# Performance work log

Measured on AMD Instinct MI355X. Metric: run time of the kernel, lower is better.

The kernel has to match this reference:

```python
import jax, jax.numpy as jnp
import numpy as np
import math

Q, D, M_KEYS, U, DELTA = 32, 64, 4096, 64, 16
B = 1024
GAMMA_ALPHA = 0.1
EPS = 1e-12


def _l2norm(v, axis):
    n = jnp.sqrt(jnp.sum(v * v, axis=axis, keepdims=True))
    return v / jnp.maximum(n, EPS)


def setup_inputs() -> dict:
    key = jax.random.key(0)
    kx, kk, km = jax.random.split(key, 3)
    x = jax.random.normal(kx, (B, D), dtype=jnp.float32)
    K = jax.random.normal(kk, (Q, M_KEYS, D), dtype=jnp.float32)
    M = jax.random.normal(km, (Q, M_KEYS, U), dtype=jnp.float32)
    return {"x": x, "K": K, "M": M}


def reference(x, K, M):
    b = x.shape[0]
    # psi: identity projection onto key space + L2 normalization
    x_bd = _l2norm(x, axis=1)                      # [b, d]
    # keys are L2-normalized along the key dimension (F.normalize, dim=2)
    Kn = _l2norm(K, axis=2)                        # [q, m, d]
    # per-neuron key matching: [b, q, m]
    responses_bqm = jnp.einsum("bd,qmd->bqm", x_bd, Kn)
    # top-delta attention responses (sorted, largest)
    top_resp_bqk, top_idx_bqk = jax.lax.top_k(responses_bqm, DELTA)
    # temperature-scaled softmax over the top-delta responses
    top_alpha_bqk = jax.nn.softmax(
        (GAMMA_ALPHA / math.sqrt(D)) * top_resp_bqk, axis=2
    )
    # gather the top-delta memory units per (batch, neuron): [b, q, k, u]
    q_idx = jnp.arange(Q)[None, :, None]           # [1, q, 1]
    top_M_bqku = M[q_idx, top_idx_bqk]             # advanced indexing gather
    # softmax-weighted combine: [b, q, u]
    W_bqu = jnp.einsum("bqk,bqku->bqu", top_alpha_bqk, top_M_bqku)
    return W_bqu
```

## Files before the change

### kernel.cpp

```cpp
#include <hip/hip_runtime.h>
#include <math.h>

#define QN 32
#define DN 64
#define MN 4096
#define UN 64
#define BN 1024
#define NDELTA 16
#define SEGS 2
#define SEGK (MN / SEGS)
#define SURV_CAP 64
#define THETA 0.27f
#define BAND  8e-3f

typedef short v8s __attribute__((ext_vector_type(8)));
typedef float v4f __attribute__((ext_vector_type(4)));

static __device__ __forceinline__ unsigned short f2bf(float f) {
    unsigned int u = __float_as_uint(f);
    unsigned int r = (u + 0x7FFF + ((u >> 16) & 1)) >> 16;
    return (unsigned short)r;
}

#define NKBLK ((QN * MN) / 16)
__global__ __launch_bounds__(256) void k_prep(const float* __restrict__ K,
                                              const float* __restrict__ x,
                                              float* __restrict__ rinvK,
                                              float* __restrict__ rinvx,
                                              unsigned short* __restrict__ Khat,
                                              unsigned short* __restrict__ xhat) {
    const int tid = threadIdx.x;
    const bool isK = blockIdx.x < NKBLK;
    const int rb   = isK ? blockIdx.x : (blockIdx.x - NKBLK);
    const int row  = rb * 16 + (tid >> 4);
    const int sub  = tid & 15;
    const float* src = isK ? K : x;
    float* rdst      = isK ? rinvK : rinvx;
    unsigned short* hdst = isK ? Khat : xhat;

    const float4* r4 = (const float4*)(src + (size_t)row * DN);
    float4 v = r4[sub];
    float ss = v.x * v.x + v.y * v.y + v.z * v.z + v.w * v.w;
    ss += __shfl_xor(ss, 1, 16);
    ss += __shfl_xor(ss, 2, 16);
    ss += __shfl_xor(ss, 4, 16);
    ss += __shfl_xor(ss, 8, 16);
    const float rinv = 1.0f / fmaxf(sqrtf(ss), 1e-12f);
    if (sub == 0) rdst[row] = rinv;
    ushort4 o;
    o.x = f2bf(v.x * rinv); o.y = f2bf(v.y * rinv);
    o.z = f2bf(v.z * rinv); o.w = f2bf(v.w * rinv);
    *(ushort4*)(hdst + (size_t)row * DN + sub * 4) = o;
}

__global__ __launch_bounds__(256, 4) void k_prefsel(
        const unsigned short* __restrict__ Khat,
        const unsigned short* __restrict__ xhat,
        unsigned int* __restrict__ cand2,
        int* __restrict__ cnt2) {
    __shared__ unsigned short sK[2][64][72];

    const int tid  = threadIdx.x;
    const int w    = tid >> 6;
    const int lane = tid & 63;

    const int d    = blockIdx.x;
    const int xcd  = d & 7;
    const int j    = d >> 3;
    const int g    = xcd + ((j >> 4) << 3);
    const int i    = j & 15;
    const int q    = g >> 1;
    const int seg  = g & 1;
    const int b0   = i * 64 + w * 16;

    const int col  = lane & 15;
    const int gg   = lane >> 4;

    const v8s* xp = (const v8s*)(xhat + (size_t)(b0 + col) * DN + gg * 8);
    const v8s xb0 = xp[0];
    const v8s xb1 = xp[4];

    const unsigned short* Kq16 = Khat + ((size_t)q * MN + seg * SEGK) * DN;
    const unsigned long long colmask = 0x0001000100010001ull << col;
    const size_t rowoff = (((size_t)(b0 + col) * QN + q) * SEGS + seg) * SURV_CAP;
    int cnt = 0;

    const int r0i = tid >> 3;
    const int oi  = (tid & 7) * 8;
    uint4 p0 = *(const uint4*)(Kq16 + (size_t)r0i * DN + oi);
    uint4 p1 = *(const uint4*)(Kq16 + (size_t)(32 + r0i) * DN + oi);
    int cur = 0;

    const int NST = SEGK / 64;
    for (int st = 0; st < NST; ++st) {
        *(uint4*)(&sK[cur][r0i][oi]) = p0;
        *(uint4*)(&sK[cur][32 + r0i][oi]) = p1;
        __syncthreads();
        if (st < NST - 1) {
            p0 = *(const uint4*)(Kq16 + (size_t)((st + 1) * 64 + r0i) * DN + oi);
            p1 = *(const uint4*)(Kq16 + (size_t)((st + 1) * 64 + 32 + r0i) * DN + oi);
        }

#pragma unroll
        for (int t2 = 0; t2 < 4; ++t2) {
            const unsigned short* arow = &sK[cur][t2 * 16 + col][0];
            const v8s a0 = *(const v8s*)(arow + gg * 8);
            const v8s a1 = *(const v8s*)(arow + gg * 8 + 32);
            v4f acc = {0.f, 0.f, 0.f, 0.f};
            acc = __builtin_amdgcn_mfma_f32_16x16x32_bf16(a0, xb0, acc, 0, 0, 0);
            acc = __builtin_amdgcn_mfma_f32_16x16x32_bf16(a1, xb1, acc, 0, 0, 0);
            const int keybase = seg * SEGK + st * 64 + t2 * 16 + gg * 4;
#pragma unroll
            for (int r = 0; r < 4; ++r) {
                const bool qual = acc[r] > THETA;
                const unsigned long long mm = __ballot(qual);
                if (mm) {
                    const unsigned long long mc = mm & colmask;
                    const int rank = __builtin_amdgcn_mbcnt_hi(
                        (unsigned int)(mc >> 32),
                        __builtin_amdgcn_mbcnt_lo((unsigned int)mc, 0));
                    const int inc = __popcll(mc);
                    if (qual) {
                        const int pos = cnt + rank;
                        if (pos < SURV_CAP)
                            cand2[rowoff + pos] =
                                (unsigned int)(keybase + r) |
                                ((unsigned int)f2bf(acc[r]) << 16);
                    }
                    cnt += inc;
                }
            }
        }
        cur ^= 1;
    }

    if (gg == 0)
        cnt2[((b0 + col) * QN + q) * SEGS + seg] = cnt < SURV_CAP ? cnt : SURV_CAP;
}

__global__ __launch_bounds__(256) void k_rescore7(
        const float* __restrict__ x,
        const float* __restrict__ K,
        const float* __restrict__ rinvx,
        const float* __restrict__ rinvK,
        const unsigned int* __restrict__ cand2,
        const int* __restrict__ cnt2,
        const float* __restrict__ Mm,
        float* __restrict__ out) {
    __shared__ float2 slist[4][NDELTA];

    const int tid  = threadIdx.x;
    const int lane = tid & 63;
    const int w    = tid >> 6;
    const unsigned long long below = (1ull << lane) - 1ull;

    const int d    = blockIdx.x;
    const int xcd  = d & 7;
    const int j    = d >> 3;
    const int q    = xcd + ((j >> 8) << 3);
    const int b    = (j & 255) * 4 + w;
    const int p    = b * QN + q;

    const int n0 = cnt2[p * SEGS + 0];
    const int n1 = cnt2[p * SEGS + 1];
    const unsigned int* cp = cand2 + (size_t)p * SEGS * SURV_CAP;
    const unsigned int eraw  = cp[lane];
    const unsigned int eraw2 = cp[SURV_CAP + lane];
    const float rx = rinvx[b];

    if (lane < NDELTA) slist[w][lane] = make_float2(0.f, 0.f);

    const bool va = lane < n0;
    const bool vb = lane < n1;
    const int key  = (int)(eraw  & 0xFFFFu);
    const int key2 = (int)(eraw2 & 0xFFFFu);
    const float m  = va ? __uint_as_float(eraw  & 0xFFFF0000u) : -INFINITY;
    const float m2 = vb ? __uint_as_float(eraw2 & 0xFFFF0000u) : -INFINITY;

    float lo = 0.25f, bh = 0.60f;
#pragma unroll
    for (int it = 0; it < 7; ++it) {
        const float tm = 0.5f * (lo + bh);
        const int c = __popcll(__ballot(m > tm)) + __popcll(__ballot(m2 > tm));
        if (c >= NDELTA) lo = tm; else bh = tm;
    }

    const bool hi  = m  > lo + BAND;
    const bool hi2 = m2 > lo + BAND;
    const bool bd  = va && !hi  && (m  >= lo - BAND);
    const bool bd2 = vb && !hi2 && (m2 >= lo - BAND);
    const unsigned long long bhi  = __ballot(hi);
    const unsigned long long bhi2 = __ballot(hi2);
    const int n_hi0 = __popcll(bhi);
    const int n_hi  = n_hi0 + __popcll(bhi2);
    const int need  = NDELTA - n_hi;

    const float4* xrow = (const float4*)(x + (size_t)b * DN);
    const float* Kq  = K + (size_t)q * MN * DN;
    const float* rKq = rinvK + (size_t)q * MN;

    float f = -INFINITY, g2 = -INFINITY;
    if (bd) {
        const float4* kr = (const float4*)(Kq + (size_t)key * DN);
        float a0 = 0.f, a1 = 0.f, a2 = 0.f, a3 = 0.f;
#pragma unroll
        for (int i = 0; i < 16; ++i) {
            const float4 xv = xrow[i];
            const float4 kv = kr[i];
            a0 = fmaf(kv.x, xv.x, a0);
            a1 = fmaf(kv.y, xv.y, a1);
            a2 = fmaf(kv.z, xv.z, a2);
            a3 = fmaf(kv.w, xv.w, a3);
        }
        f = ((a0 + a1) + (a2 + a3)) * (rx * rKq[key]);
    }
    const unsigned long long bbd2 = __ballot(bd2);
    if (bbd2) {
        if (bd2) {
            const float4* kr = (const float4*)(Kq + (size_t)key2 * DN);
            float a0 = 0.f, a1 = 0.f, a2 = 0.f, a3 = 0.f;
#pragma unroll
            for (int i = 0; i < 16; ++i) {
                const float4 xv = xrow[i];
                const float4 kv = kr[i];
                a0 = fmaf(kv.x, xv.x, a0);
                a1 = fmaf(kv.y, xv.y, a1);
                a2 = fmaf(kv.z, xv.z, a2);
                a3 = fmaf(kv.w, xv.w, a3);
            }
            g2 = ((a0 + a1) + (a2 + a3)) * (rx * rKq[key2]);
        }
    }

    int rkf = 0, rkf2 = 0;
    unsigned long long t1m = __ballot(bd);
    while (t1m) {
        const int t = __ffsll(t1m) - 1; t1m &= t1m - 1;
        const float ft = __shfl(f, t);
        const int   kt = __shfl(key, t);
        rkf  += (ft > f  || (ft == f  && kt < key )) ? 1 : 0;
        rkf2 += (ft > g2 || (ft == g2 && kt < key2)) ? 1 : 0;
    }
    unsigned long long t2m = bbd2;
    while (t2m) {
        const int t = __ffsll(t2m) - 1; t2m &= t2m - 1;
        const float ft = __shfl(g2, t);
        const int   kt = __shfl(key2, t);
        rkf  += (ft > f  || (ft == f  && kt < key )) ? 1 : 0;
        rkf2 += (ft > g2 || (ft == g2 && kt < key2)) ? 1 : 0;
    }

    const float SM_SCALE = (float)(0.1 / 8.0);
    if (hi)
        slist[w][__popcll(bhi & below)] =
            make_float2(__expf(m * SM_SCALE) , __int_as_float(key));
    if (hi2)
        slist[w][n_hi0 + __popcll(bhi2 & below)] =
            make_float2(__expf(m2 * SM_SCALE), __int_as_float(key2));
    if (bd && rkf < need)
        slist[w][n_hi + rkf] =
            make_float2(__expf(f * SM_SCALE) , __int_as_float(key));
    if (bd2 && rkf2 < need)
        slist[w][n_hi + rkf2] =
            make_float2(__expf(g2 * SM_SCALE), __int_as_float(key2));

    const float2 mine = slist[w][lane & 15];
    const float* Mq = Mm + (size_t)q * MN * UN;
    float ssum = 0.f;
    float acc = 0.f;
#pragma unroll
    for (int t = 0; t < NDELTA; ++t) {
        const float e  = __shfl(mine.x, t);
        const int   id = __float_as_int(__shfl(mine.y, t));
        ssum += e;
        acc = fmaf(e, Mq[(size_t)id * UN + lane], acc);
    }
    const float rs = ssum > 0.f ? 1.0f / ssum : 0.f;
    out[(size_t)p * UN + lane] = acc * rs;
}

extern "C" void kernel_launch(void* const* d_in, const int* in_sizes, int n_in,
                              void* d_out, int out_size, void* d_ws, size_t ws_size,
                              hipStream_t stream) {
    const float* x  = (const float*)d_in[0];
    const float* K  = (const float*)d_in[1];
    const float* Mm = (const float*)d_in[2];
    float* out = (float*)d_out;

    char* wsb = (char*)d_ws;
    float* rinvK = (float*)wsb;                   wsb += (size_t)QN * MN * 4;
    float* rinvx = (float*)wsb;                   wsb += (size_t)BN * 4;
    int*   cnt2  = (int*)wsb;                     wsb += (size_t)BN * QN * SEGS * 4;
    unsigned short* Khat = (unsigned short*)wsb;  wsb += (size_t)QN * MN * DN * 2;
    unsigned short* xhat = (unsigned short*)wsb;  wsb += (size_t)BN * DN * 2;
    unsigned int* cand2 = (unsigned int*)wsb;

    k_prep    <<<dim3(NKBLK + BN / 16), 256, 0, stream>>>(K, x, rinvK, rinvx,
                                                          Khat, xhat);
    k_prefsel <<<dim3(1024), 256, 0, stream>>>(Khat, xhat, cand2, cnt2);
    k_rescore7<<<dim3((BN * QN) / 4), 256, 0, stream>>>(x, K, rinvx, rinvK,
                                                        cand2, cnt2, Mm, out);
}
```

Baseline: 230.5 us.

## Fuse prefilter and rescore kernels, keeping candidate lists in shared memory

Merges the bf16 MFMA prefilter and the exact rescore/gather kernels into one kernel. Each block now scans all 4096 keys of a neuron for 64 batch rows and keeps up to 128 candidates per row in LDS, so the global candidate and count buffers and one launch go away. The cost is half as many blocks (512) and a large LDS footprint (about 32KB for candidates), which lowers occupancy. The rescore work is also serialized, with each wave looping over 16 rows, so parallelism and latency hiding may drop.

```diff
diff --git a/kernel.cpp b/kernel.cpp
--- a/kernel.cpp
+++ b/kernel.cpp
@@ -7,9 +7,7 @@
 #define UN 64
 #define BN 1024
 #define NDELTA 16
-#define SEGS 2
-#define SEGK (MN / SEGS)
-#define SURV_CAP 64
+#define CAP 128
 #define THETA 0.27f
 #define BAND  8e-3f
 
@@ -53,36 +51,40 @@
     *(ushort4*)(hdst + (size_t)row * DN + sub * 4) = o;
 }
 
-__global__ __launch_bounds__(256, 4) void k_prefsel(
+__global__ __launch_bounds__(256) void k_fused(
         const unsigned short* __restrict__ Khat,
         const unsigned short* __restrict__ xhat,
-        unsigned int* __restrict__ cand2,
-        int* __restrict__ cnt2) {
+        const float* __restrict__ x,
+        const float* __restrict__ K,
+        const float* __restrict__ rinvx,
+        const float* __restrict__ rinvK,
+        const float* __restrict__ Mm,
+        float* __restrict__ out) {
     __shared__ unsigned short sK[2][64][72];
+    __shared__ unsigned int clist[64][CAP];
+    __shared__ float2 slist[4][NDELTA];
 
     const int tid  = threadIdx.x;
     const int w    = tid >> 6;
     const int lane = tid & 63;
 
-    const int d    = blockIdx.x;
-    const int xcd  = d & 7;
-    const int j    = d >> 3;
-    const int g    = xcd + ((j >> 4) << 3);
-    const int i    = j & 15;
-    const int q    = g >> 1;
-    const int seg  = g & 1;
-    const int b0   = i * 64 + w * 16;
-
-    const int col  = lane & 15;
-    const int gg   = lane >> 4;
+    const int d   = blockIdx.x;
+    const int xcd = d & 7;
+    const int j   = d >> 3;
+    const int q   = xcd + ((j >> 4) << 3);
+    const int i   = j & 15;
+    const int b0  = i * 64 + w * 16;
+
+    const int col = lane & 15;
+    const int gg  = lane >> 4;
 
     const v8s* xp = (const v8s*)(xhat + (size_t)(b0 + col) * DN + gg * 8);
     const v8s xb0 = xp[0];
     const v8s xb1 = xp[4];
 
-    const unsigned short* Kq16 = Khat + ((size_t)q * MN + seg * SEGK) * DN;
+    const unsigned short* Kq16 = Khat + (size_t)q * MN * DN;
     const unsigned long long colmask = 0x0001000100010001ull << col;
-    const size_t rowoff = (((size_t)(b0 + col) * QN + q) * SEGS + seg) * SURV_CAP;
+    const int lb0 = w * 16 + col;
     int cnt = 0;
 
     const int r0i = tid >> 3;
@@ -91,7 +93,7 @@
     uint4 p1 = *(const uint4*)(Kq16 + (size_t)(32 + r0i) * DN + oi);
     int cur = 0;
 
-    const int NST = SEGK / 64;
+    const int NST = MN / 64;
     for (int st = 0; st < NST; ++st) {
         *(uint4*)(&sK[cur][r0i][oi]) = p0;
         *(uint4*)(&sK[cur][32 + r0i][oi]) = p1;
@@ -109,7 +111,7 @@
             v4f acc = {0.f, 0.f, 0.f, 0.f};
             acc = __builtin_amdgcn_mfma_f32_16x16x32_bf16(a0, xb0, acc, 0, 0, 0);
             acc = __builtin_amdgcn_mfma_f32_16x16x32_bf16(a1, xb1, acc, 0, 0, 0);
-            const int keybase = seg * SEGK + st * 64 + t2 * 16 + gg * 4;
+            const int keybase = st * 64 + t2 * 16 + gg * 4;
 #pragma unroll
             for (int r = 0; r < 4; ++r) {
                 const bool qual = acc[r] > THETA;
@@ -122,8 +124,8 @@
                     const int inc = __popcll(mc);
                     if (qual) {
                         const int pos = cnt + rank;
-                        if (pos < SURV_CAP)
-                            cand2[rowoff + pos] =
+                        if (pos < CAP)
+                            clist[lb0][pos] =
                                 (unsigned int)(keybase + r) |
                                 ((unsigned int)f2bf(acc[r]) << 16);
                     }
@@ -134,149 +136,133 @@
         cur ^= 1;
     }
 
-    if (gg == 0)
-        cnt2[((b0 + col) * QN + q) * SEGS + seg] = cnt < SURV_CAP ? cnt : SURV_CAP;
-}
-
-__global__ __launch_bounds__(256) void k_rescore7(
-        const float* __restrict__ x,
-        const float* __restrict__ K,
-        const float* __restrict__ rinvx,
-        const float* __restrict__ rinvK,
-        const unsigned int* __restrict__ cand2,
-        const int* __restrict__ cnt2,
-        const float* __restrict__ Mm,
-        float* __restrict__ out) {
-    __shared__ float2 slist[4][NDELTA];
-
-    const int tid  = threadIdx.x;
-    const int lane = tid & 63;
-    const int w    = tid >> 6;
-    const unsigned long long below = (1ull << lane) - 1ull;
-
-    const int d    = blockIdx.x;
-    const int xcd  = d & 7;
-    const int j    = d >> 3;
-    const int q    = xcd + ((j >> 8) << 3);
-    const int b    = (j & 255) * 4 + w;
-    const int p    = b * QN + q;
-
-    const int n0 = cnt2[p * SEGS + 0];
-    const int n1 = cnt2[p * SEGS + 1];
-    const unsigned int* cp = cand2 + (size_t)p * SEGS * SURV_CAP;
-    const unsigned int eraw  = cp[lane];
-    const unsigned int eraw2 = cp[SURV_CAP + lane];
-    const float rx = rinvx[b];
-
-    if (lane < NDELTA) slist[w][lane] = make_float2(0.f, 0.f);
-
-    const bool va = lane < n0;
-    const bool vb = lane < n1;
-    const int key  = (int)(eraw  & 0xFFFFu);
-    const int key2 = (int)(eraw2 & 0xFFFFu);
-    const float m  = va ? __uint_as_float(eraw  & 0xFFFF0000u) : -INFINITY;
-    const float m2 = vb ? __uint_as_float(eraw2 & 0xFFFF0000u) : -INFINITY;
-
-    float lo = 0.25f, bh = 0.60f;
-#pragma unroll
-    for (int it = 0; it < 7; ++it) {
-        const float tm = 0.5f * (lo + bh);
-        const int c = __popcll(__ballot(m > tm)) + __popcll(__ballot(m2 > tm));
-        if (c >= NDELTA) lo = tm; else bh = tm;
-    }
-
-    const bool hi  = m  > lo + BAND;
-    const bool hi2 = m2 > lo + BAND;
-    const bool bd  = va && !hi  && (m  >= lo - BAND);
-    const bool bd2 = vb && !hi2 && (m2 >= lo - BAND);
-    const unsigned long long bhi  = __ballot(hi);
-    const unsigned long long bhi2 = __ballot(hi2);
-    const int n_hi0 = __popcll(bhi);
-    const int n_hi  = n_hi0 + __popcll(bhi2);
-    const int need  = NDELTA - n_hi;
-
-    const float4* xrow = (const float4*)(x + (size_t)b * DN);
     const float* Kq  = K + (size_t)q * MN * DN;
     const float* rKq = rinvK + (size_t)q * MN;
-
-    float f = -INFINITY, g2 = -INFINITY;
-    if (bd) {
-        const float4* kr = (const float4*)(Kq + (size_t)key * DN);
-        float a0 = 0.f, a1 = 0.f, a2 = 0.f, a3 = 0.f;
-#pragma unroll
-        for (int i = 0; i < 16; ++i) {
-            const float4 xv = xrow[i];
-            const float4 kv = kr[i];
-            a0 = fmaf(kv.x, xv.x, a0);
-            a1 = fmaf(kv.y, xv.y, a1);
-            a2 = fmaf(kv.z, xv.z, a2);
-            a3 = fmaf(kv.w, xv.w, a3);
-        }
-        f = ((a0 + a1) + (a2 + a3)) * (rx * rKq[key]);
-    }
-    const unsigned long long bbd2 = __ballot(bd2);
-    if (bbd2) {
-        if (bd2) {
-            const float4* kr = (const float4*)(Kq + (size_t)key2 * DN);
+    const float* Mq  = Mm + (size_t)q * MN * UN;
+    const unsigned long long below = (1ull << lane) - 1ull;
+    const float SM_SCALE = (float)(0.1 / 8.0);
+
+#pragma unroll 1
+    for (int it = 0; it < 16; ++it) {
+        const int bb = b0 + it;
+        const int lb = w * 16 + it;
+        const int p  = bb * QN + q;
+
+        int n = __shfl(cnt, it);
+        n = n < CAP ? n : CAP;
+        const int n0 = n < 64 ? n : 64;
+        const int n1 = n - n0;
+
+        const unsigned int eraw  = clist[lb][lane];
+        const unsigned int eraw2 = clist[lb][64 + lane];
+        const float rx = rinvx[bb];
+
+        if (lane < NDELTA) slist[w][lane] = make_float2(0.f, 0.f);
+
+        const bool va = lane < n0;
+        const bool vb = lane < n1;
+        const int key  = (int)(eraw  & 0xFFFFu);
+        const int key2 = (int)(eraw2 & 0xFFFFu);
+        const float m  = va ? __uint_as_float(eraw  & 0xFFFF0000u) : -INFINITY;
+        const float m2 = vb ? __uint_as_float(eraw2 & 0xFFFF0000u) : -INFINITY;
+
+        float lo = 0.25f, bh = 0.60f;
+#pragma unroll
+        for (int s = 0; s < 7; ++s) {
+            const float tm = 0.5f * (lo + bh);
+            const int c = __popcll(__ballot(m > tm)) + __popcll(__ballot(m2 > tm));
+            if (c >= NDELTA) lo = tm; else bh = tm;
+        }
+
+        const bool hi  = m  > lo + BAND;
+        const bool hi2 = m2 > lo + BAND;
+        const bool bd  = va && !hi  && (m  >= lo - BAND);
+        const bool bd2 = vb && !hi2 && (m2 >= lo - BAND);
+        const unsigned long long bhi  = __ballot(hi);
+        const unsigned long long bhi2 = __ballot(hi2);
+        const int n_hi0 = __popcll(bhi);
+        const int n_hi  = n_hi0 + __popcll(bhi2);
+        const int need  = NDELTA - n_hi;
+
+        const float4* xrow = (const float4*)(x + (size_t)bb * DN);
+
+        float f = -INFINITY, g2 = -INFINITY;
+        if (bd) {
+            const float4* kr = (const float4*)(Kq + (size_t)key * DN);
             float a0 = 0.f, a1 = 0.f, a2 = 0.f, a3 = 0.f;
 #pragma unroll
-            for (int i = 0; i < 16; ++i) {
-                const float4 xv = xrow[i];
-                const float4 kv = kr[i];
+            for (int k4 = 0; k4 < 16; ++k4) {
+                const float4 xv = xrow[k4];
+                const float4 kv = kr[k4];
                 a0 = fmaf(kv.x, xv.x, a0);
                 a1 = fmaf(kv.y, xv.y, a1);
                 a2 = fmaf(kv.z, xv.z, a2);
                 a3 = fmaf(kv.w, xv.w, a3);
             }
-            g2 = ((a0 + a1) + (a2 + a3)) * (rx * rKq[key2]);
-        }
+            f = ((a0 + a1) + (a2 + a3)) * (rx * rKq[key]);
+        }
+        const unsigned long long bbd2 = __ballot(bd2);
+        if (bbd2) {
+            if (bd2) {
+                const float4* kr = (const float4*)(Kq + (size_t)key2 * DN);
+                float a0 = 0.f, a1 = 0.f, a2 = 0.f, a3 = 0.f;
+#pragma unroll
+                for (int k4 = 0; k4 < 16; ++k4) {
+                    const float4 xv = xrow[k4];
+                    const float4 kv = kr[k4];
+                    a0 = fmaf(kv.x, xv.x, a0);
+                    a1 = fmaf(kv.y, xv.y, a1);
+                    a2 = fmaf(kv.z, xv.z, a2);
+                    a3 = fmaf(kv.w, xv.w, a3);
+                }
+                g2 = ((a0 + a1) + (a2 + a3)) * (rx * rKq[key2]);
+            }
+        }
+
+        int rkf = 0, rkf2 = 0;
+        unsigned long long t1m = __ballot(bd);
+        while (t1m) {
+            const int t = __ffsll(t1m) - 1; t1m &= t1m - 1;
+            const float ft = __shfl(f, t);
+            const int   kt = __shfl(key, t);
+            rkf  += (ft > f  || (ft == f  && kt < key )) ? 1 : 0;
+            rkf2 += (ft > g2 || (ft == g2 && kt < key2)) ? 1 : 0;
+        }
+        unsigned long long t2m = bbd2;
+        while (t2m) {
+            const int t = __ffsll(t2m) - 1; t2m &= t2m - 1;
+            const float ft = __shfl(g2, t);
+            const int   kt = __shfl(key2, t);
+            rkf  += (ft > f  || (ft == f  && kt < key )) ? 1 : 0;
+            rkf2 += (ft > g2 || (ft == g2 && kt < key2)) ? 1 : 0;
+        }
+
+        if (hi)
+            slist[w][__popcll(bhi & below)] =
+                make_float2(__expf(m * SM_SCALE) , __int_as_float(key));
+        if (hi2)
+            slist[w][n_hi0 + __popcll(bhi2 & below)] =
+                make_float2(__expf(m2 * SM_SCALE), __int_as_float(key2));
+        if (bd && rkf < need)
+            slist[w][n_hi + rkf] =
+                make_float2(__expf(f * SM_SCALE) , __int_as_float(key));
+        if (bd2 && rkf2 < need)
+            slist[w][n_hi + rkf2] =
+                make_float2(__expf(g2 * SM_SCALE), __int_as_float(key2));
+
+        const float2 mine = slist[w][lane & 15];
+        float ssum = 0.f;
+        float acc = 0.f;
+#pragma unroll
+        for (int t = 0; t < NDELTA; ++t) {
+            const float e  = __shfl(mine.x, t);
+            const int   id = __float_as_int(__shfl(mine.y, t));
+            ssum += e;
+            acc = fmaf(e, Mq[(size_t)id * UN + lane], acc);
+        }
+        const float rs = ssum > 0.f ? 1.0f / ssum : 0.f;
+        out[(size_t)p * UN + lane] = acc * rs;
     }
-
-    int rkf = 0, rkf2 = 0;
-    unsigned long long t1m = __ballot(bd);
-    while (t1m) {
-        const int t = __ffsll(t1m) - 1; t1m &= t1m - 1;
-        const float ft = __shfl(f, t);
-        const int   kt = __shfl(key, t);
-        rkf  += (ft > f  || (ft == f  && kt < key )) ? 1 : 0;
-        rkf2 += (ft > g2 || (ft == g2 && kt < key2)) ? 1 : 0;
-    }
-    unsigned long long t2m = bbd2;
-    while (t2m) {
-        const int t = __ffsll(t2m) - 1; t2m &= t2m - 1;
-        const float ft = __shfl(g2, t);
-        const int   kt = __shfl(key2, t);
-        rkf  += (ft > f  || (ft == f  && kt < key )) ? 1 : 0;
-        rkf2 += (ft > g2 || (ft == g2 && kt < key2)) ? 1 : 0;
-    }
-
-    const float SM_SCALE = (float)(0.1 / 8.0);
-    if (hi)
-        slist[w][__popcll(bhi & below)] =
-            make_float2(__expf(m * SM_SCALE) , __int_as_float(key));
-    if (hi2)
-        slist[w][n_hi0 + __popcll(bhi2 & below)] =
-            make_float2(__expf(m2 * SM_SCALE), __int_as_float(key2));
-    if (bd && rkf < need)
-        slist[w][n_hi + rkf] =
-            make_float2(__expf(f * SM_SCALE) , __int_as_float(key));
-    if (bd2 && rkf2 < need)
-        slist[w][n_hi + rkf2] =
-            make_float2(__expf(g2 * SM_SCALE), __int_as_float(key2));
-
-    const float2 mine = slist[w][lane & 15];
-    const float* Mq = Mm + (size_t)q * MN * UN;
-    float ssum = 0.f;
-    float acc = 0.f;
-#pragma unroll
-    for (int t = 0; t < NDELTA; ++t) {
-        const float e  = __shfl(mine.x, t);
-        const int   id = __float_as_int(__shfl(mine.y, t));
-        ssum += e;
-        acc = fmaf(e, Mq[(size_t)id * UN + lane], acc);
-    }
-    const float rs = ssum > 0.f ? 1.0f / ssum : 0.f;
-    out[(size_t)p * UN + lane] = acc * rs;
 }
 
 extern "C" void kernel_launch(void* const* d_in, const int* in_sizes, int n_in,
@@ -290,14 +276,11 @@
     char* wsb = (char*)d_ws;
     float* rinvK = (float*)wsb;                   wsb += (size_t)QN * MN * 4;
     float* rinvx = (float*)wsb;                   wsb += (size_t)BN * 4;
-    int*   cnt2  = (int*)wsb;                     wsb += (size_t)BN * QN * SEGS * 4;
     unsigned short* Khat = (unsigned short*)wsb;  wsb += (size_t)QN * MN * DN * 2;
-    unsigned short* xhat = (unsigned short*)wsb;  wsb += (size_t)BN * DN * 2;
-    unsigned int* cand2 = (unsigned int*)wsb;
-
-    k_prep    <<<dim3(NKBLK + BN / 16), 256, 0, stream>>>(K, x, rinvK, rinvx,
-                                                          Khat, xhat);
-    k_prefsel <<<dim3(1024), 256, 0, stream>>>(Khat, xhat, cand2, cnt2);
-    k_rescore7<<<dim3((BN * QN) / 4), 256, 0, stream>>>(x, K, rinvx, rinvK,
-                                                        cand2, cnt2, Mm, out);
-}
+    unsigned short* xhat = (unsigned short*)wsb;
+
+    k_prep <<<dim3(NKBLK + BN / 16), 256, 0, stream>>>(K, x, rinvK, rinvx,
+                                                       Khat, xhat);
+    k_fused<<<dim3(512), 256, 0, stream>>>(Khat, xhat, x, K, rinvx, rinvK,
+                                           Mm, out);
+}
```

Result: slower. 256.1 us (+11.1%).
